# Kernel tuning notes

Measured on AMD Instinct MI355X. Metric: run time of the kernel, lower is better.

The kernel has to match this reference:

```python
import jax, jax.numpy as jnp
import numpy as np

B, S, H = 16, 4096, 1152
GRID = 64  # 64x64 patch grid -> S = GRID*GRID
OUT_LEN = 256  # pooled soft tokens (k = sqrt(S/OUT_LEN) = 4)


def setup_inputs() -> dict:
    key = jax.random.key(0)
    x = jax.random.normal(key, (B, S, H), dtype=jnp.float32)
    i = jnp.arange(S)
    # position_ids[..., 0] = x coord, [..., 1] = y coord on the patch grid
    pos = jnp.stack([i % GRID, i // GRID], axis=-1).astype(jnp.int32)  # [S, 2]
    position_ids = jnp.broadcast_to(pos, (B, S, 2))
    return {"x": x, "position_ids": position_ids, "output_length": OUT_LEN}


def reference(x, position_ids, output_length):
    b, s, h = x.shape
    # zero out padding positions (pos == [-1, -1])
    padding = jnp.all(position_ids == -1, axis=-1)  # [B, S]
    x = jnp.where(padding[..., None], jnp.float32(0.0), x)

    k = int((s // output_length) ** 0.5)
    k2 = k * k

    pos = jnp.maximum(position_ids, 0)
    max_x = jnp.max(pos[..., 0], axis=-1, keepdims=True) + 1  # [B, 1]
    # bucket index of each patch: (x//k) + (max_x//k) * (y//k)
    kidx = pos[..., 0] // k + (max_x // k) * pos[..., 1] // 1 * 0 + (pos[..., 0] // k) * 0 + (pos[..., 0] // k)
    kidx = pos[..., 0] // k + (max_x // k) * (pos[..., 1] // k)  # [B, S]

    # scatter-mean: segment_sum over flattened (batch-offset) bucket ids, / k^2
    seg = (kidx + jnp.arange(b)[:, None] * output_length).reshape(-1)
    pooled = jax.ops.segment_sum(
        x.reshape(b * s, h), seg, num_segments=b * output_length
    ).reshape(b, output_length, h) / jnp.float32(k2)

    root_hidden = jnp.float32(h ** 0.5)
    return pooled * root_hidden
```

## Files before the change

kernel.cpp:

```cpp
#include <hip/hip_runtime.h>


#define BB 16
#define SS 4096
#define HH 1152
#define OUTL 256
#define KK 4
#define K2 16
#define H4 (HH / 4)

__global__ __launch_bounds__(256) void maxx_kernel(const int* __restrict__ pos,
                                                   int* __restrict__ maxx) {
    int b = blockIdx.x;
    int t = threadIdx.x;
    int m = 0;
    for (int s = t; s < SS; s += 256) {
        int px = pos[((size_t)b * SS + s) * 2];
        if (px > m) m = px;
    }
    __shared__ int red[256];
    red[t] = m;
    __syncthreads();
    for (int w = 128; w > 0; w >>= 1) {
        if (t < w) red[t] = max(red[t], red[t + w]);
        __syncthreads();
    }
    if (t == 0) maxx[b] = red[0] + 1;
}

__global__ __launch_bounds__(256) void build_kernel(const int* __restrict__ pos,
                                                    const int* __restrict__ maxx,
                                                    int* __restrict__ counts,
                                                    int* __restrict__ rows) {
    int idx = blockIdx.x * 256 + threadIdx.x;
    if (idx >= BB * SS) return;
    int b = idx / SS, s = idx % SS;
    int px = pos[(size_t)idx * 2];
    int py = pos[(size_t)idx * 2 + 1];
    if (px == -1 && py == -1) return;
    px = max(px, 0);
    py = max(py, 0);
    int mx = maxx[b];
    int kidx = px / KK + (mx / KK) * (py / KK);
    if (kidx < 0 || kidx >= OUTL) return;
    int slot = atomicAdd(&counts[b * OUTL + kidx], 1);
    if (slot < K2) rows[((size_t)b * OUTL + kidx) * K2 + slot] = s;
}

__global__ __launch_bounds__(256) void gather_kernel(const float* __restrict__ x,
                                                     const int* __restrict__ counts,
                                                     const int* __restrict__ rows,
                                                     float* __restrict__ out) {
    int idx = blockIdx.x * 256 + threadIdx.x;
    int c = idx % H4;
    int bo = idx / H4;
    int b = bo / OUTL;
    const float4* x4 = reinterpret_cast<const float4*>(x) + (size_t)b * SS * H4;
    int cnt = counts[bo];
    if (cnt > K2) cnt = K2;
    const int* rl = rows + (size_t)bo * K2;
    float4 acc = {0.f, 0.f, 0.f, 0.f};
    if (cnt == K2) {
#pragma unroll
        for (int j = 0; j < K2; ++j) {
            int row = rl[j];
            float4 v = x4[(size_t)row * H4 + c];
            acc.x += v.x; acc.y += v.y; acc.z += v.z; acc.w += v.w;
        }
    } else {
        for (int j = 0; j < cnt; ++j) {
            int row = rl[j];
            float4 v = x4[(size_t)row * H4 + c];
            acc.x += v.x; acc.y += v.y; acc.z += v.z; acc.w += v.w;
        }
    }
    const float scale = 33.94112549695428f / 16.0f;
    float4 r;
    r.x = acc.x * scale; r.y = acc.y * scale; r.z = acc.z * scale; r.w = acc.w * scale;
    reinterpret_cast<float4*>(out)[idx] = r;
}

extern "C" void kernel_launch(void* const* d_in, const int* in_sizes, int n_in,
                              void* d_out, int out_size, void* d_ws, size_t ws_size,
                              hipStream_t stream) {
    const float* x = (const float*)d_in[0];
    const int* pos = (const int*)d_in[1];
    float* out = (float*)d_out;

    int* counts = (int*)d_ws;
    int* rows = counts + BB * OUTL;
    int* maxx = rows + (size_t)BB * OUTL * K2;

    hipMemsetAsync(counts, 0, (size_t)BB * OUTL * sizeof(int), stream);

    maxx_kernel<<<BB, 256, 0, stream>>>(pos, maxx);

    int nbs = (BB * SS + 255) / 256;
    build_kernel<<<nbs, 256, 0, stream>>>(pos, maxx, counts, rows);

    int total4 = BB * OUTL * H4;
    int nbg = total4 / 256;
    gather_kernel<<<nbg, 256, 0, stream>>>(x, counts, rows, out);
}
```

Before: 72.25 us.

## Fuse max and bucket-build into one per-batch kernel with LDS atomics; widen gather

Replaces the memset, max-x kernel and global-atomic build kernel with a single per-batch block that computes max x, buckets rows using shared-memory atomics, and writes counts and row lists out. This removes two launches, the memset, and global atomic contention. The gather kernel now handles two float4 columns per thread, halving thread count and adding memory-level parallelism per thread. The fused build runs only 16 blocks, so its serial loop over 4096 positions per block could lengthen the build phase. Because rows are now written from shared memory, their order within a bucket changes, which may slightly alter summation order.

Result: faster. 64.98 us (-10.1%).

```diff
diff --git a/kernel.cpp b/kernel.cpp
--- a/kernel.cpp
+++ b/kernel.cpp
@@ -8,14 +8,18 @@
 #define KK 4
 #define K2 16
 #define H4 (HH / 4)
+#define HP (H4 / 2)
 
-__global__ __launch_bounds__(256) void maxx_kernel(const int* __restrict__ pos,
-                                                   int* __restrict__ maxx) {
+__global__ __launch_bounds__(256) void build_fused(const int* __restrict__ pos,
+                                                   int* __restrict__ counts,
+                                                   int* __restrict__ rows) {
     int b = blockIdx.x;
     int t = threadIdx.x;
+    const int2* p2 = reinterpret_cast<const int2*>(pos) + (size_t)b * SS;
+
     int m = 0;
     for (int s = t; s < SS; s += 256) {
-        int px = pos[((size_t)b * SS + s) * 2];
+        int px = p2[s].x;
         if (px > m) m = px;
     }
     __shared__ int red[256];
@@ -25,26 +29,29 @@
         if (t < w) red[t] = max(red[t], red[t + w]);
         __syncthreads();
     }
-    if (t == 0) maxx[b] = red[0] + 1;
-}
+    __shared__ int smx;
+    if (t == 0) smx = red[0] + 1;
 
-__global__ __launch_bounds__(256) void build_kernel(const int* __restrict__ pos,
-                                                    const int* __restrict__ maxx,
-                                                    int* __restrict__ counts,
-                                                    int* __restrict__ rows) {
-    int idx = blockIdx.x * 256 + threadIdx.x;
-    if (idx >= BB * SS) return;
-    int b = idx / SS, s = idx % SS;
-    int px = pos[(size_t)idx * 2];
-    int py = pos[(size_t)idx * 2 + 1];
-    if (px == -1 && py == -1) return;
-    px = max(px, 0);
-    py = max(py, 0);
-    int mx = maxx[b];
-    int kidx = px / KK + (mx / KK) * (py / KK);
-    if (kidx < 0 || kidx >= OUTL) return;
-    int slot = atomicAdd(&counts[b * OUTL + kidx], 1);
-    if (slot < K2) rows[((size_t)b * OUTL + kidx) * K2 + slot] = s;
+    __shared__ int lcnt[OUTL];
+    __shared__ int lrows[OUTL * K2];
+    lcnt[t] = 0;
+    __syncthreads();
+    int mxk = smx / KK;
+    for (int s = t; s < SS; s += 256) {
+        int2 xy = p2[s];
+        if (xy.x == -1 && xy.y == -1) continue;
+        int px = max(xy.x, 0), py = max(xy.y, 0);
+        int kidx = px / KK + mxk * (py / KK);
+        if ((unsigned)kidx < OUTL) {
+            int slot = atomicAdd(&lcnt[kidx], 1);
+            if (slot < K2) lrows[kidx * K2 + slot] = s;
+        }
+    }
+    __syncthreads();
+
+    counts[b * OUTL + t] = lcnt[t];
+    int* rb = rows + (size_t)b * OUTL * K2;
+    for (int i = t; i < OUTL * K2; i += 256) rb[i] = lrows[i];
 }
 
 __global__ __launch_bounds__(256) void gather_kernel(const float* __restrict__ x,
@@ -52,32 +59,41 @@
                                                      const int* __restrict__ rows,
                                                      float* __restrict__ out) {
     int idx = blockIdx.x * 256 + threadIdx.x;
-    int c = idx % H4;
-    int bo = idx / H4;
+    int c2 = idx % HP;
+    int bo = idx / HP;
     int b = bo / OUTL;
-    const float4* x4 = reinterpret_cast<const float4*>(x) + (size_t)b * SS * H4;
+    int col = c2 * 2;
+
+    const float4* x4 = reinterpret_cast<const float4*>(x) + (size_t)b * SS * H4 + col;
+    const int* rl = rows + (size_t)bo * K2;
     int cnt = counts[bo];
     if (cnt > K2) cnt = K2;
-    const int* rl = rows + (size_t)bo * K2;
-    float4 acc = {0.f, 0.f, 0.f, 0.f};
+
+    float4 a0 = {0.f, 0.f, 0.f, 0.f};
+    float4 a1 = {0.f, 0.f, 0.f, 0.f};
     if (cnt == K2) {
 #pragma unroll
         for (int j = 0; j < K2; ++j) {
-            int row = rl[j];
-            float4 v = x4[(size_t)row * H4 + c];
-            acc.x += v.x; acc.y += v.y; acc.z += v.z; acc.w += v.w;
+            const float4* p = x4 + (size_t)rl[j] * H4;
+            float4 v0 = p[0], v1 = p[1];
+            a0.x += v0.x; a0.y += v0.y; a0.z += v0.z; a0.w += v0.w;
+            a1.x += v1.x; a1.y += v1.y; a1.z += v1.z; a1.w += v1.w;
         }
     } else {
         for (int j = 0; j < cnt; ++j) {
-            int row = rl[j];
-            float4 v = x4[(size_t)row * H4 + c];
-            acc.x += v.x; acc.y += v.y; acc.z += v.z; acc.w += v.w;
+            const float4* p = x4 + (size_t)rl[j] * H4;
+            float4 v0 = p[0], v1 = p[1];
+            a0.x += v0.x; a0.y += v0.y; a0.z += v0.z; a0.w += v0.w;
+            a1.x += v1.x; a1.y += v1.y; a1.z += v1.z; a1.w += v1.w;
         }
     }
-    const float scale = 33.94112549695428f / 16.0f;
-    float4 r;
-    r.x = acc.x * scale; r.y = acc.y * scale; r.z = acc.z * scale; r.w = acc.w * scale;
-    reinterpret_cast<float4*>(out)[idx] = r;
+    const float scale = 2.1213203435596424f;
+    float4 r0, r1;
+    r0.x = a0.x * scale; r0.y = a0.y * scale; r0.z = a0.z * scale; r0.w = a0.w * scale;
+    r1.x = a1.x * scale; r1.y = a1.y * scale; r1.z = a1.z * scale; r1.w = a1.w * scale;
+    float4* o4 = reinterpret_cast<float4*>(out) + (size_t)bo * H4 + col;
+    o4[0] = r0;
+    o4[1] = r1;
 }
 
 extern "C" void kernel_launch(void* const* d_in, const int* in_sizes, int n_in,
@@ -89,16 +105,9 @@
 
     int* counts = (int*)d_ws;
     int* rows = counts + BB * OUTL;
-    int* maxx = rows + (size_t)BB * OUTL * K2;
 
-    hipMemsetAsync(counts, 0, (size_t)BB * OUTL * sizeof(int), stream);
+    build_fused<<<BB, 256, 0, stream>>>(pos, counts, rows);
 
-    maxx_kernel<<<BB, 256, 0, stream>>>(pos, maxx);
-
-    int nbs = (BB * SS + 255) / 256;
-    build_kernel<<<nbs, 256, 0, stream>>>(pos, maxx, counts, rows);
-
-    int total4 = BB * OUTL * H4;
-    int nbg = total4 / 256;
-    gather_kernel<<<nbg, 256, 0, stream>>>(x, counts, rows, out);
+    int total = BB * OUTL * HP;
+    gather_kernel<<<total / 256, 256, 0, stream>>>(x, counts, rows, out);
 }
```
